# Performance work log

Hardware: AMD Instinct MI355X
Metric: run time of the kernel (lower is better)

The kernel has to match this reference:

```python
import jax, jax.numpy as jnp
import numpy as np

N_NODES = 100000
N_EDGES = 1600000
IN_F = 256
OUT_F = 128


def setup_inputs() -> dict:
    key = jax.random.key(0)
    k1, k2, k3, k4, k5, k6 = jax.random.split(key, 6)
    x = jax.random.normal(k1, (N_NODES, IN_F), dtype=jnp.float32)
    edge_row = jax.random.randint(k2, (N_EDGES,), 0, N_NODES, dtype=jnp.int32)
    edge_col = jax.random.randint(k3, (N_EDGES,), 0, N_NODES, dtype=jnp.int32)
    edge_val = jax.random.uniform(k4, (N_EDGES,), dtype=jnp.float32)
    # xavier_uniform for W: bound = sqrt(6/(fan_in+fan_out))
    bound_w = float(np.sqrt(6.0 / (IN_F + OUT_F)))
    W = jax.random.uniform(k5, (IN_F, OUT_F), dtype=jnp.float32, minval=-bound_w, maxval=bound_w)
    stdv = 1.0 / float(np.sqrt(OUT_F))
    b = jax.random.uniform(k6, (OUT_F,), dtype=jnp.float32, minval=-stdv, maxval=stdv)
    return {"x": x, "edge_row": edge_row, "edge_col": edge_col, "edge_val": edge_val, "W": W, "b": b}


def reference(x, edge_row, edge_col, edge_val, W, b):
    # dropout p=0.0 -> identity
    support = x @ W + b                      # [N, out]
    # sparse adjacency matmul: out[r] += val * support[c] over edges (r, c, val)
    msgs = edge_val[:, None] * support[edge_col]          # [E, out]
    out = jax.ops.segment_sum(msgs, edge_row, num_segments=N_NODES)  # [N, out]
    return jax.nn.relu(out)
```

## Files before the change

kernel.cpp:

```cpp
#include <hip/hip_runtime.h>


constexpr int kNodes = 100000;
constexpr int kEdges = 1600000;
constexpr int kInF   = 256;
constexpr int kOutF  = 128;
constexpr int kTiles = kNodes / 16;
constexpr int kBucketBlocks = 800;
constexpr int kGemmBlocks = 1250;

constexpr int kNB = 256;
constexpr int kRB = 391;
constexpr int kCap = 7424;
constexpr int kTileCap = 1024;

typedef __attribute__((ext_vector_type(8))) short short8;
typedef __attribute__((ext_vector_type(8))) unsigned short ush8;
typedef __attribute__((ext_vector_type(4))) float floatx4;

__device__ inline unsigned short f2bf_rne(float f) {
    unsigned int u = __float_as_uint(f);
    unsigned int r = u + 0x7FFFu + ((u >> 16) & 1u);
    return (unsigned short)(r >> 16);
}
__device__ inline float bf2f(unsigned short h) {
    return __uint_as_float(((unsigned int)h) << 16);
}

__device__ inline short8 cvt8_bf16(const float4 a, const float4 b) {
    union { short8 s; unsigned int u[4]; } r;
    asm("v_cvt_pk_bf16_f32 %0, %1, %2" : "=v"(r.u[0]) : "v"(a.x), "v"(a.y));
    asm("v_cvt_pk_bf16_f32 %0, %1, %2" : "=v"(r.u[1]) : "v"(a.z), "v"(a.w));
    asm("v_cvt_pk_bf16_f32 %0, %1, %2" : "=v"(r.u[2]) : "v"(b.x), "v"(b.y));
    asm("v_cvt_pk_bf16_f32 %0, %1, %2" : "=v"(r.u[3]) : "v"(b.z), "v"(b.w));
    return r.s;
}

__device__ inline void gload_lds16(const void* g, void* l) {
    __builtin_amdgcn_global_load_lds(
        (const __attribute__((address_space(1))) unsigned int*)g,
        (__attribute__((address_space(3))) unsigned int*)l,
        16, 0, 0);
}

__global__ __launch_bounds__(256) void gcn_gemm(const float* __restrict__ x,
                                                const float* __restrict__ W,
                                                const float* __restrict__ b,
                                                unsigned short* __restrict__ support) {
    __shared__ __align__(16) float lbuf[2][4096];

    const int lane = threadIdx.x & 63;
    const int wv   = threadIdx.x >> 6;
    const int rowl = lane & 15;
    const int quad = lane >> 4;
    const int colbase = wv * 32;

    short8 bfrag[2][8];
#pragma unroll
    for (int ct = 0; ct < 2; ++ct) {
        const int col = colbase + ct * 16 + rowl;
#pragma unroll
        for (int kc = 0; kc < 8; ++kc) {
            const int kb = kc * 32 + quad * 8;
            short8 f;
#pragma unroll
            for (int j = 0; j < 8; ++j)
                f[j] = (short)f2bf_rne(W[(size_t)(kb + j) * kOutF + col]);
            bfrag[ct][kc] = f;
        }
    }
    const float bias0 = b[colbase + rowl];
    const float bias1 = b[colbase + 16 + rowl];

    const int G = gridDim.x;
    int t = blockIdx.x;

#define GEMM_STAGE(buf_, tile_)                                                   \
    do {                                                                          \
        const float* tb_ = x + (size_t)(tile_) * 16 * kInF;                       \
        _Pragma("unroll")                                                         \
        for (int i_ = 0; i_ < 4; ++i_) {                                          \
            const int row_ = i_ * 4 + wv;                                         \
            gload_lds16(tb_ + (size_t)row_ * kInF + ((lane ^ (row_ & 7)) << 2),   \
                        &lbuf[buf_][row_ << 8]);                                  \
        }                                                                         \
    } while (0)

    if (t < kTiles) GEMM_STAGE(0, t);
    int cur = 0;

    for (; t < kTiles; t += G) {
        const int tn = t + G;
        asm volatile("s_waitcnt vmcnt(0)" ::: "memory");
        __syncthreads();
        if (tn < kTiles) GEMM_STAGE(cur ^ 1, tn);

        const int r0 = t * 16;
        const float* base = &lbuf[cur][rowl << 8];
        const int rsw = rowl & 7;
        floatx4 acc0 = {0.f, 0.f, 0.f, 0.f};
        floatx4 acc1 = {0.f, 0.f, 0.f, 0.f};
#pragma unroll
        for (int kc = 0; kc < 8; ++kc) {
            const int g0 = (kc << 3) + (quad << 1);
            const float4 v0 = *reinterpret_cast<const float4*>(base + ((g0 ^ rsw) << 2));
            const float4 v1 = *reinterpret_cast<const float4*>(base + (((g0 + 1) ^ rsw) << 2));
            const short8 a = cvt8_bf16(v0, v1);
            acc0 = __builtin_amdgcn_mfma_f32_16x16x32_bf16(a, bfrag[0][kc], acc0, 0, 0, 0);
            acc1 = __builtin_amdgcn_mfma_f32_16x16x32_bf16(a, bfrag[1][kc], acc1, 0, 0, 0);
        }
#pragma unroll
        for (int reg = 0; reg < 4; ++reg) {
            const size_t rbase = (size_t)(r0 + quad * 4 + reg) * kOutF + colbase;
            support[rbase + rowl]      = f2bf_rne(acc0[reg] + bias0);
            support[rbase + 16 + rowl] = f2bf_rne(acc1[reg] + bias1);
        }
        cur ^= 1;
    }
#undef GEMM_STAGE
}

__global__ __launch_bounds__(256) void gcn_bhist(const int* __restrict__ erow,
                                                 int* __restrict__ bucket_tot) {
    __shared__ int cnt[kNB];
    cnt[threadIdx.x] = 0;
    __syncthreads();
    const int stride = gridDim.x * blockDim.x;
    for (int e = blockIdx.x * blockDim.x + threadIdx.x; e < kEdges; e += stride)
        atomicAdd(&cnt[(unsigned int)erow[e] / (unsigned int)kRB], 1);
    __syncthreads();
    const int c = cnt[threadIdx.x];
    if (c) atomicAdd(&bucket_tot[threadIdx.x], c);
}

__global__ __launch_bounds__(256) void gcn_bscan(const int* __restrict__ bucket_tot,
                                                 int* __restrict__ bucket_base,
                                                 int* __restrict__ bucket_cursor,
                                                 int* __restrict__ row_start) {
    __shared__ int s[256];
    const int v = bucket_tot[threadIdx.x];
    s[threadIdx.x] = v;
    __syncthreads();
#pragma unroll
    for (int off = 1; off < 256; off <<= 1) {
        const int t = (threadIdx.x >= off) ? s[threadIdx.x - off] : 0;
        __syncthreads();
        s[threadIdx.x] += t;
        __syncthreads();
    }
    const int excl = s[threadIdx.x] - v;
    bucket_base[threadIdx.x]   = excl;
    bucket_cursor[threadIdx.x] = excl;
    if (threadIdx.x == 255) {
        bucket_base[256]   = kEdges;
        row_start[kNodes]  = kEdges;
    }
}

__global__ __launch_bounds__(256) void gcn_bin(const int* __restrict__ erow,
                                               const int* __restrict__ ecol,
                                               const float* __restrict__ eval,
                                               int* __restrict__ bucket_cursor,
                                               int2* __restrict__ packed) {
    __shared__ int cnt[kNB];
    __shared__ int base[kNB];
    __shared__ int rk[kNB];
    const int T   = kBucketBlocks * 256;
    const int tid = blockIdx.x * 256 + threadIdx.x;

    cnt[threadIdx.x] = 0;
    rk[threadIdx.x]  = 0;

    int bk[8], pk[8], vb[8];
    bool ok[8];
#pragma unroll
    for (int i = 0; i < 8; ++i) {
        const int e = tid + i * T;
        ok[i] = (e < kEdges);
        const int r = ok[i] ? erow[e] : 0;
        const int c = ok[i] ? ecol[e] : 0;
        const float v = ok[i] ? eval[e] : 0.f;
        const unsigned int b = (unsigned int)r / (unsigned int)kRB;
        bk[i] = (int)b;
        pk[i] = ((r - (int)b * kRB) << 17) | c;
        vb[i] = __float_as_int(v);
    }
    __syncthreads();
#pragma unroll
    for (int i = 0; i < 8; ++i)
        if (ok[i]) atomicAdd(&cnt[bk[i]], 1);
    __syncthreads();
    const int c = cnt[threadIdx.x];
    base[threadIdx.x] = c ? atomicAdd(&bucket_cursor[threadIdx.x], c) : 0;
    __syncthreads();
#pragma unroll
    for (int i = 0; i < 8; ++i) {
        if (ok[i]) {
            const int r = atomicAdd(&rk[bk[i]], 1);
            packed[base[bk[i]] + r] = make_int2(pk[i], vb[i]);
        }
    }
}

__global__ __launch_bounds__(256) void gcn_place(const int* __restrict__ bucket_base,
                                                 int* __restrict__ row_start,
                                                 int2* __restrict__ packed) {
    __shared__ int2 st[kCap];
    __shared__ int  s[512];
    __shared__ int  rcur[kRB + 1];
    const int bk = blockIdx.x;
    const int r0 = bk * kRB;
    const int r1 = min(r0 + kRB, kNodes);
    const int NR = r1 - r0;
    if (NR <= 0) return;
    const int bb = bucket_base[bk];
    const int s1 = bucket_base[bk + 1];
    const int size   = s1 - bb;
    const int staged = min(size, kCap);
    const int tid = threadIdx.x;

    s[tid] = 0;
    s[tid + 256] = 0;
    __syncthreads();

    for (int i = tid; i < staged; i += 256) {
        const int2 p = packed[bb + i];
        st[i] = p;
        atomicAdd(&s[p.x >> 17], 1);
    }
    int2 tail[8];
    int  nt = 0;
    for (int i = kCap + tid; i < size; i += 256) {
        if (nt < 8) {
            tail[nt] = packed[bb + i];
            atomicAdd(&s[tail[nt].x >> 17], 1);
            ++nt;
        }
    }
    __syncthreads();

    const int i0 = tid, i1 = tid + 256;
#pragma unroll
    for (int off = 1; off < 512; off <<= 1) {
        const int v0 = (i0 >= off) ? s[i0 - off] : 0;
        const int v1 = (i1 >= off) ? s[i1 - off] : 0;
        __syncthreads();
        s[i0] += v0;
        s[i1] += v1;
        __syncthreads();
    }

    for (int i = tid; i < NR; i += 256) {
        const int excl = i ? s[i - 1] : 0;
        row_start[r0 + i] = bb + excl;
        rcur[i] = excl;
    }
    __syncthreads();

    for (int i = tid; i < staged; i += 256) {
        const int2 p  = st[i];
        const int pos = bb + atomicAdd(&rcur[p.x >> 17], 1);
        packed[pos] = make_int2(p.x & 0x1FFFF, p.y);
    }
#pragma unroll
    for (int t = 0; t < 8; ++t) {
        if (t < nt) {
            const int2 p  = tail[t];
            const int pos = bb + atomicAdd(&rcur[p.x >> 17], 1);
            packed[pos] = make_int2(p.x & 0x1FFFF, p.y);
        }
    }
}

__global__ __launch_bounds__(256) void gcn_aggregate(const int* __restrict__ row_start,
                                                     const int2* __restrict__ packed,
                                                     const unsigned short* __restrict__ support,
                                                     float* __restrict__ out) {
    __shared__ int2 ep[kTileCap];
    const int n0 = blockIdx.x * 16;
    const int e0 = row_start[n0];
    const int eN = row_start[n0 + 16] - e0;
    const int nStage = min(eN, kTileCap);
    for (int i = threadIdx.x; i < nStage; i += 256)
        ep[i] = packed[e0 + i];
    __syncthreads();

    const int n  = n0 + (threadIdx.x >> 4);
    const int f8 = (threadIdx.x & 15) * 8;
    const unsigned short* sb = support + f8;
    const int s0 = row_start[n]     - e0;
    const int s1 = row_start[n + 1] - e0;

    float acc[8];
#pragma unroll
    for (int j = 0; j < 8; ++j) acc[j] = 0.f;

    if (eN <= kTileCap) {
        int i = s0;
        for (; i + 7 < s1; i += 8) {
            int2 p[8];
#pragma unroll
            for (int k = 0; k < 8; ++k) p[k] = ep[i + k];
            ush8 g[8];
#pragma unroll
            for (int k = 0; k < 8; ++k)
                g[k] = *reinterpret_cast<const ush8*>(sb + (size_t)p[k].x * kOutF);
#pragma unroll
            for (int k = 0; k < 8; ++k) {
                const float v = __int_as_float(p[k].y);
#pragma unroll
                for (int j = 0; j < 8; ++j) acc[j] += v * bf2f(g[k][j]);
            }
        }
        for (; i < s1; ++i) {
            const int2 p = ep[i];
            const float v = __int_as_float(p.y);
            const ush8 g = *reinterpret_cast<const ush8*>(sb + (size_t)p.x * kOutF);
#pragma unroll
            for (int j = 0; j < 8; ++j) acc[j] += v * bf2f(g[j]);
        }
    } else {
        int i = s0;
        for (; i + 3 < s1; i += 4) {
            const int2 p0 = packed[e0 + i];
            const int2 p1 = packed[e0 + i + 1];
            const int2 p2 = packed[e0 + i + 2];
            const int2 p3 = packed[e0 + i + 3];
            const ush8 a0 = *reinterpret_cast<const ush8*>(sb + (size_t)p0.x * kOutF);
            const ush8 a1 = *reinterpret_cast<const ush8*>(sb + (size_t)p1.x * kOutF);
            const ush8 a2 = *reinterpret_cast<const ush8*>(sb + (size_t)p2.x * kOutF);
            const ush8 a3 = *reinterpret_cast<const ush8*>(sb + (size_t)p3.x * kOutF);
            const float v0 = __int_as_float(p0.y), v1 = __int_as_float(p1.y);
            const float v2 = __int_as_float(p2.y), v3 = __int_as_float(p3.y);
#pragma unroll
            for (int j = 0; j < 8; ++j) {
                acc[j] += v0 * bf2f(a0[j]);
                acc[j] += v1 * bf2f(a1[j]);
                acc[j] += v2 * bf2f(a2[j]);
                acc[j] += v3 * bf2f(a3[j]);
            }
        }
        for (; i < s1; ++i) {
            const int2 p = packed[e0 + i];
            const float v = __int_as_float(p.y);
            const ush8 a = *reinterpret_cast<const ush8*>(sb + (size_t)p.x * kOutF);
#pragma unroll
            for (int j = 0; j < 8; ++j) acc[j] += v * bf2f(a[j]);
        }
    }

    float4 o0 = make_float4(fmaxf(acc[0], 0.f), fmaxf(acc[1], 0.f),
                            fmaxf(acc[2], 0.f), fmaxf(acc[3], 0.f));
    float4 o1 = make_float4(fmaxf(acc[4], 0.f), fmaxf(acc[5], 0.f),
                            fmaxf(acc[6], 0.f), fmaxf(acc[7], 0.f));
    *reinterpret_cast<float4*>(out + (size_t)n * kOutF + f8)     = o0;
    *reinterpret_cast<float4*>(out + (size_t)n * kOutF + f8 + 4) = o1;
}

extern "C" void kernel_launch(void* const* d_in, const int* in_sizes, int n_in,
                              void* d_out, int out_size, void* d_ws, size_t ws_size,
                              hipStream_t stream) {
    const float* x    = (const float*)d_in[0];
    const int*   erow = (const int*)  d_in[1];
    const int*   ecol = (const int*)  d_in[2];
    const float* eval = (const float*)d_in[3];
    const float* W    = (const float*)d_in[4];
    const float* b    = (const float*)d_in[5];
    float* out = (float*)d_out;

    char* ws = (char*)d_ws;
    unsigned short* support = (unsigned short*)(ws);
    int2* packed        = (int2*)(ws + 25600000);
    int*  row_start     = (int*) (ws + 38400000);
    int*  bucket_tot    = (int*) (ws + 38800008);
    int*  bucket_base   = (int*) (ws + 38801032);
    int*  bucket_cursor = (int*) (ws + 38802060);

    gcn_gemm<<<kGemmBlocks, 256, 0, stream>>>(x, W, b, support);

    hipMemsetAsync(bucket_tot, 0, kNB * sizeof(int), stream);
    gcn_bhist<<<1024, 256, 0, stream>>>(erow, bucket_tot);
    gcn_bscan<<<1, 256, 0, stream>>>(bucket_tot, bucket_base, bucket_cursor, row_start);
    gcn_bin  <<<kBucketBlocks, 256, 0, stream>>>(erow, ecol, eval, bucket_cursor, packed);
    gcn_place<<<kNB, 256, 0, stream>>>(bucket_base, row_start, packed);

    gcn_aggregate<<<kTiles, 256, 0, stream>>>(row_start, packed, support, out);
}
```

Baseline: 349.0 us.

## Fuse CSR build into one cooperative kernel with grid syncs and finer buckets

Replaces the four CSR-construction kernels (bucket histogram, scan, bin, place) with one cooperative kernel. It uses grid-wide syncs between the count, scatter and per-bucket placement phases, so erow is read once and kept in registers. Buckets are made finer (768 buckets of 131 rows) so each block owns one bucket and stages it in a smaller LDS buffer. This removes several launch gaps and one pass over erow, in exchange for grid.sync overhead and a requirement that all 768 blocks be co-resident.

```diff
diff --git a/kernel.cpp b/kernel.cpp
--- a/kernel.cpp
+++ b/kernel.cpp
@@ -1,4 +1,7 @@
 #include <hip/hip_runtime.h>
+#include <hip/hip_cooperative_groups.h>
+
+namespace cg = cooperative_groups;
 
 
 constexpr int kNodes = 100000;
@@ -6,12 +9,14 @@
 constexpr int kInF   = 256;
 constexpr int kOutF  = 128;
 constexpr int kTiles = kNodes / 16;
-constexpr int kBucketBlocks = 800;
 constexpr int kGemmBlocks = 1250;
 
-constexpr int kNB = 256;
-constexpr int kRB = 391;
-constexpr int kCap = 7424;
+constexpr int kNB  = 768;
+constexpr int kRB  = 131;
+constexpr int kCap = 2432;
+constexpr int kCsrBlocks = kNB;
+constexpr int kEPB = (kEdges + kCsrBlocks - 1) / kCsrBlocks;
+
 constexpr int kTileCap = 1024;
 
 typedef __attribute__((ext_vector_type(8))) short short8;
@@ -120,153 +125,131 @@
 #undef GEMM_STAGE
 }
 
-__global__ __launch_bounds__(256) void gcn_bhist(const int* __restrict__ erow,
-                                                 int* __restrict__ bucket_tot) {
-    __shared__ int cnt[kNB];
-    cnt[threadIdx.x] = 0;
-    __syncthreads();
-    const int stride = gridDim.x * blockDim.x;
-    for (int e = blockIdx.x * blockDim.x + threadIdx.x; e < kEdges; e += stride)
-        atomicAdd(&cnt[(unsigned int)erow[e] / (unsigned int)kRB], 1);
-    __syncthreads();
-    const int c = cnt[threadIdx.x];
-    if (c) atomicAdd(&bucket_tot[threadIdx.x], c);
-}
-
-__global__ __launch_bounds__(256) void gcn_bscan(const int* __restrict__ bucket_tot,
-                                                 int* __restrict__ bucket_base,
-                                                 int* __restrict__ bucket_cursor,
-                                                 int* __restrict__ row_start) {
-    __shared__ int s[256];
-    const int v = bucket_tot[threadIdx.x];
-    s[threadIdx.x] = v;
-    __syncthreads();
-#pragma unroll
-    for (int off = 1; off < 256; off <<= 1) {
-        const int t = (threadIdx.x >= off) ? s[threadIdx.x - off] : 0;
+__global__ __launch_bounds__(256, 3) void gcn_csr(const int* __restrict__ erow,
+                                                  const int* __restrict__ ecol,
+                                                  const float* __restrict__ eval,
+                                                  int* __restrict__ cursor_rel,
+                                                  int2* __restrict__ packed,
+                                                  int* __restrict__ row_start) {
+    __shared__ int2 st[kCap];
+    __shared__ int  cnt[kNB];
+    __shared__ int  rk[kNB];
+    __shared__ int  s2[kNB];
+    const int tid = threadIdx.x;
+    const int blk = blockIdx.x;
+    cg::grid_group grid = cg::this_grid();
+
+    const int eb0 = blk * kEPB;
+    const int eb1 = min(eb0 + kEPB, kEdges);
+
+    for (int i = tid; i < kNB; i += 256) { cnt[i] = 0; rk[i] = 0; }
+    __syncthreads();
+    unsigned int bkrl[9];
+#pragma unroll
+    for (int i = 0; i < 9; ++i) {
+        const int e = eb0 + i * 256 + tid;
+        bkrl[i] = 0xFFFFFFFFu;
+        if (e < eb1) {
+            const int r = erow[e];
+            const unsigned int bk = (unsigned int)r / (unsigned int)kRB;
+            bkrl[i] = (bk << 8) | (unsigned int)(r - (int)bk * kRB);
+            atomicAdd(&cnt[bk], 1);
+        }
+    }
+    __syncthreads();
+    for (int i = tid; i < kNB; i += 256) {
+        const int c = cnt[i];
+        cnt[i] = c ? atomicAdd(&cursor_rel[i], c) : 0;
+    }
+    __threadfence();
+    grid.sync();
+
+    {
+        for (int j = 0; j < 3; ++j) s2[tid + j * 256] = cursor_rel[tid + j * 256];
         __syncthreads();
-        s[threadIdx.x] += t;
-        __syncthreads();
-    }
-    const int excl = s[threadIdx.x] - v;
-    bucket_base[threadIdx.x]   = excl;
-    bucket_cursor[threadIdx.x] = excl;
-    if (threadIdx.x == 255) {
-        bucket_base[256]   = kEdges;
-        row_start[kNodes]  = kEdges;
-    }
-}
-
-__global__ __launch_bounds__(256) void gcn_bin(const int* __restrict__ erow,
-                                               const int* __restrict__ ecol,
-                                               const float* __restrict__ eval,
-                                               int* __restrict__ bucket_cursor,
-                                               int2* __restrict__ packed) {
-    __shared__ int cnt[kNB];
-    __shared__ int base[kNB];
-    __shared__ int rk[kNB];
-    const int T   = kBucketBlocks * 256;
-    const int tid = blockIdx.x * 256 + threadIdx.x;
-
-    cnt[threadIdx.x] = 0;
-    rk[threadIdx.x]  = 0;
-
-    int bk[8], pk[8], vb[8];
-    bool ok[8];
-#pragma unroll
-    for (int i = 0; i < 8; ++i) {
-        const int e = tid + i * T;
-        ok[i] = (e < kEdges);
-        const int r = ok[i] ? erow[e] : 0;
-        const int c = ok[i] ? ecol[e] : 0;
-        const float v = ok[i] ? eval[e] : 0.f;
-        const unsigned int b = (unsigned int)r / (unsigned int)kRB;
-        bk[i] = (int)b;
-        pk[i] = ((r - (int)b * kRB) << 17) | c;
-        vb[i] = __float_as_int(v);
-    }
-    __syncthreads();
-#pragma unroll
-    for (int i = 0; i < 8; ++i)
-        if (ok[i]) atomicAdd(&cnt[bk[i]], 1);
-    __syncthreads();
-    const int c = cnt[threadIdx.x];
-    base[threadIdx.x] = c ? atomicAdd(&bucket_cursor[threadIdx.x], c) : 0;
-    __syncthreads();
-#pragma unroll
-    for (int i = 0; i < 8; ++i) {
-        if (ok[i]) {
-            const int r = atomicAdd(&rk[bk[i]], 1);
-            packed[base[bk[i]] + r] = make_int2(pk[i], vb[i]);
-        }
-    }
-}
-
-__global__ __launch_bounds__(256) void gcn_place(const int* __restrict__ bucket_base,
-                                                 int* __restrict__ row_start,
-                                                 int2* __restrict__ packed) {
-    __shared__ int2 st[kCap];
-    __shared__ int  s[512];
-    __shared__ int  rcur[kRB + 1];
-    const int bk = blockIdx.x;
-    const int r0 = bk * kRB;
+        for (int off = 1; off < kNB; off <<= 1) {
+            int v0 = 0, v1 = 0, v2 = 0;
+            if (tid        >= off) v0 = s2[tid        - off];
+            if (tid + 256  >= off) v1 = s2[tid + 256  - off];
+            if (tid + 512  >= off) v2 = s2[tid + 512  - off];
+            __syncthreads();
+            s2[tid]       += v0;
+            s2[tid + 256] += v1;
+            s2[tid + 512] += v2;
+            __syncthreads();
+        }
+    }
+    const int inclb = s2[blk];
+    const int sbase = blk ? s2[blk - 1] : 0;
+    const int ssize = inclb - sbase;
+    for (int i = tid; i < kNB; i += 256)
+        cnt[i] += (i ? s2[i - 1] : 0);
+    __syncthreads();
+
+#pragma unroll
+    for (int i = 0; i < 9; ++i) {
+        const int e = eb0 + i * 256 + tid;
+        if (e < eb1) {
+            const unsigned int br = bkrl[i];
+            const int bk = (int)(br >> 8);
+            const int rl = (int)(br & 0xFFu);
+            const int c  = ecol[e];
+            const float v = eval[e];
+            const int pos = cnt[bk] + atomicAdd(&rk[bk], 1);
+            packed[pos] = make_int2((rl << 17) | c, __float_as_int(v));
+        }
+    }
+    __threadfence();
+    grid.sync();
+
+    const int r0 = blk * kRB;
+    if (r0 >= kNodes) return;
     const int r1 = min(r0 + kRB, kNodes);
     const int NR = r1 - r0;
-    if (NR <= 0) return;
-    const int bb = bucket_base[bk];
-    const int s1 = bucket_base[bk + 1];
-    const int size   = s1 - bb;
-    const int staged = min(size, kCap);
-    const int tid = threadIdx.x;
-
-    s[tid] = 0;
-    s[tid + 256] = 0;
-    __syncthreads();
-
+    const int staged = min(ssize, kCap);
+
+    s2[tid] = 0;
+    __syncthreads();
     for (int i = tid; i < staged; i += 256) {
-        const int2 p = packed[bb + i];
+        const int2 p = packed[sbase + i];
         st[i] = p;
-        atomicAdd(&s[p.x >> 17], 1);
+        atomicAdd(&s2[p.x >> 17], 1);
     }
     int2 tail[8];
     int  nt = 0;
-    for (int i = kCap + tid; i < size; i += 256) {
+    for (int i = kCap + tid; i < ssize; i += 256) {
         if (nt < 8) {
-            tail[nt] = packed[bb + i];
-            atomicAdd(&s[tail[nt].x >> 17], 1);
+            tail[nt] = packed[sbase + i];
+            atomicAdd(&s2[tail[nt].x >> 17], 1);
             ++nt;
         }
     }
     __syncthreads();
 
-    const int i0 = tid, i1 = tid + 256;
-#pragma unroll
-    for (int off = 1; off < 512; off <<= 1) {
-        const int v0 = (i0 >= off) ? s[i0 - off] : 0;
-        const int v1 = (i1 >= off) ? s[i1 - off] : 0;
+    for (int off = 1; off < 256; off <<= 1) {
+        const int v = (tid >= off) ? s2[tid - off] : 0;
         __syncthreads();
-        s[i0] += v0;
-        s[i1] += v1;
+        s2[tid] += v;
         __syncthreads();
     }
-
-    for (int i = tid; i < NR; i += 256) {
-        const int excl = i ? s[i - 1] : 0;
-        row_start[r0 + i] = bb + excl;
-        rcur[i] = excl;
-    }
+    if (tid < NR) {
+        const int excl = tid ? s2[tid - 1] : 0;
+        row_start[r0 + tid] = sbase + excl;
+        rk[tid] = excl;
+    }
+    if (blk == 0 && tid == 0) row_start[kNodes] = kEdges;
     __syncthreads();
 
     for (int i = tid; i < staged; i += 256) {
         const int2 p  = st[i];
-        const int pos = bb + atomicAdd(&rcur[p.x >> 17], 1);
+        const int pos = sbase + atomicAdd(&rk[p.x >> 17], 1);
         packed[pos] = make_int2(p.x & 0x1FFFF, p.y);
     }
 #pragma unroll
     for (int t = 0; t < 8; ++t) {
         if (t < nt) {
             const int2 p  = tail[t];
-            const int pos = bb + atomicAdd(&rcur[p.x >> 17], 1);
+            const int pos = sbase + atomicAdd(&rk[p.x >> 17], 1);
             packed[pos] = make_int2(p.x & 0x1FFFF, p.y);
         }
     }
@@ -370,19 +353,17 @@
 
     char* ws = (char*)d_ws;
     unsigned short* support = (unsigned short*)(ws);
-    int2* packed        = (int2*)(ws + 25600000);
-    int*  row_start     = (int*) (ws + 38400000);
-    int*  bucket_tot    = (int*) (ws + 38800008);
-    int*  bucket_base   = (int*) (ws + 38801032);
-    int*  bucket_cursor = (int*) (ws + 38802060);
+    int2* packed     = (int2*)(ws + 25600000);
+    int*  row_start  = (int*) (ws + 38400000);
+    int*  cursor_rel = (int*) (ws + 38800008);
 
     gcn_gemm<<<kGemmBlocks, 256, 0, stream>>>(x, W, b, support);
 
-    hipMemsetAsync(bucket_tot, 0, kNB * sizeof(int), stream);
-    gcn_bhist<<<1024, 256, 0, stream>>>(erow, bucket_tot);
-    gcn_bscan<<<1, 256, 0, stream>>>(bucket_tot, bucket_base, bucket_cursor, row_start);
-    gcn_bin  <<<kBucketBlocks, 256, 0, stream>>>(erow, ecol, eval, bucket_cursor, packed);
-    gcn_place<<<kNB, 256, 0, stream>>>(bucket_base, row_start, packed);
+    hipMemsetAsync(cursor_rel, 0, kNB * sizeof(int), stream);
+    void* cargs[] = {(void*)&erow, (void*)&ecol, (void*)&eval,
+                     (void*)&cursor_rel, (void*)&packed, (void*)&row_start};
+    hipLaunchCooperativeKernel((const void*)gcn_csr, dim3(kCsrBlocks), dim3(256),
+                               cargs, 0, stream);
 
     gcn_aggregate<<<kTiles, 256, 0, stream>>>(row_start, packed, support, out);
 }
```

New measurement: 619.6 us. +77.6%, slower.

## Use finer row buckets and contiguous per-block edge ranges in binning sort

Applied to the files above, without the earlier changes.

Increases the number of row buckets from 256 to 1024 (98 rows each), so each placement block handles a smaller bucket with a smaller shared staging area and a shorter 128-entry scan. The bin kernel now gives each of 256 blocks a contiguous edge range, makes two passes (count, then scatter) instead of holding 8 edges in registers, and reads erow twice. The aim is more parallelism and better occupancy in gcn_place and more local scatter writes, at the cost of extra global reads and more global cursor atomics.

```diff
diff --git a/kernel.cpp b/kernel.cpp
--- a/kernel.cpp
+++ b/kernel.cpp
@@ -6,12 +6,14 @@
 constexpr int kInF   = 256;
 constexpr int kOutF  = 128;
 constexpr int kTiles = kNodes / 16;
-constexpr int kBucketBlocks = 800;
 constexpr int kGemmBlocks = 1250;
 
-constexpr int kNB = 256;
-constexpr int kRB = 391;
-constexpr int kCap = 7424;
+constexpr int kNB  = 1024;
+constexpr int kRB  = 98;
+constexpr int kCap = 1792;
+constexpr int kBinBlocks = 256;
+constexpr int kEPB = kEdges / kBinBlocks;
+
 constexpr int kTileCap = 1024;
 
 typedef __attribute__((ext_vector_type(8))) short short8;
@@ -123,82 +125,87 @@
 __global__ __launch_bounds__(256) void gcn_bhist(const int* __restrict__ erow,
                                                  int* __restrict__ bucket_tot) {
     __shared__ int cnt[kNB];
-    cnt[threadIdx.x] = 0;
-    __syncthreads();
-    const int stride = gridDim.x * blockDim.x;
-    for (int e = blockIdx.x * blockDim.x + threadIdx.x; e < kEdges; e += stride)
+    const int tid = threadIdx.x;
+    for (int i = tid; i < kNB; i += 256) cnt[i] = 0;
+    __syncthreads();
+    const int eb0 = blockIdx.x * kEPB;
+    const int eb1 = min(eb0 + kEPB, kEdges);
+    for (int e = eb0 + tid; e < eb1; e += 256)
         atomicAdd(&cnt[(unsigned int)erow[e] / (unsigned int)kRB], 1);
     __syncthreads();
-    const int c = cnt[threadIdx.x];
-    if (c) atomicAdd(&bucket_tot[threadIdx.x], c);
+    for (int i = tid; i < kNB; i += 256) {
+        const int c = cnt[i];
+        if (c) atomicAdd(&bucket_tot[i], c);
+    }
 }
 
 __global__ __launch_bounds__(256) void gcn_bscan(const int* __restrict__ bucket_tot,
                                                  int* __restrict__ bucket_base,
-                                                 int* __restrict__ bucket_cursor,
+                                                 int* __restrict__ cursor,
                                                  int* __restrict__ row_start) {
-    __shared__ int s[256];
-    const int v = bucket_tot[threadIdx.x];
-    s[threadIdx.x] = v;
-    __syncthreads();
-#pragma unroll
-    for (int off = 1; off < 256; off <<= 1) {
-        const int t = (threadIdx.x >= off) ? s[threadIdx.x - off] : 0;
-        __syncthreads();
-        s[threadIdx.x] += t;
-        __syncthreads();
-    }
-    const int excl = s[threadIdx.x] - v;
-    bucket_base[threadIdx.x]   = excl;
-    bucket_cursor[threadIdx.x] = excl;
-    if (threadIdx.x == 255) {
-        bucket_base[256]   = kEdges;
-        row_start[kNodes]  = kEdges;
+    __shared__ int s[kNB];
+    const int tid = threadIdx.x;
+    int t[4];
+#pragma unroll
+    for (int j = 0; j < 4; ++j) {
+        const int idx = tid + j * 256;
+        t[j] = bucket_tot[idx];
+        s[idx] = t[j];
+    }
+    __syncthreads();
+    for (int off = 1; off < kNB; off <<= 1) {
+        int v[4];
+#pragma unroll
+        for (int j = 0; j < 4; ++j) {
+            const int idx = tid + j * 256;
+            v[j] = (idx >= off) ? s[idx - off] : 0;
+        }
+        __syncthreads();
+#pragma unroll
+        for (int j = 0; j < 4; ++j) s[tid + j * 256] += v[j];
+        __syncthreads();
+    }
+#pragma unroll
+    for (int j = 0; j < 4; ++j) {
+        const int idx = tid + j * 256;
+        const int excl = s[idx] - t[j];
+        bucket_base[idx] = excl;
+        cursor[idx]      = excl;
+    }
+    if (tid == 255) {
+        bucket_base[kNB]  = kEdges;
+        row_start[kNodes] = kEdges;
     }
 }
 
 __global__ __launch_bounds__(256) void gcn_bin(const int* __restrict__ erow,
                                                const int* __restrict__ ecol,
                                                const float* __restrict__ eval,
-                                               int* __restrict__ bucket_cursor,
+                                               int* __restrict__ cursor,
                                                int2* __restrict__ packed) {
     __shared__ int cnt[kNB];
-    __shared__ int base[kNB];
     __shared__ int rk[kNB];
-    const int T   = kBucketBlocks * 256;
-    const int tid = blockIdx.x * 256 + threadIdx.x;
-
-    cnt[threadIdx.x] = 0;
-    rk[threadIdx.x]  = 0;
-
-    int bk[8], pk[8], vb[8];
-    bool ok[8];
-#pragma unroll
-    for (int i = 0; i < 8; ++i) {
-        const int e = tid + i * T;
-        ok[i] = (e < kEdges);
-        const int r = ok[i] ? erow[e] : 0;
-        const int c = ok[i] ? ecol[e] : 0;
-        const float v = ok[i] ? eval[e] : 0.f;
-        const unsigned int b = (unsigned int)r / (unsigned int)kRB;
-        bk[i] = (int)b;
-        pk[i] = ((r - (int)b * kRB) << 17) | c;
-        vb[i] = __float_as_int(v);
-    }
-    __syncthreads();
-#pragma unroll
-    for (int i = 0; i < 8; ++i)
-        if (ok[i]) atomicAdd(&cnt[bk[i]], 1);
-    __syncthreads();
-    const int c = cnt[threadIdx.x];
-    base[threadIdx.x] = c ? atomicAdd(&bucket_cursor[threadIdx.x], c) : 0;
-    __syncthreads();
-#pragma unroll
-    for (int i = 0; i < 8; ++i) {
-        if (ok[i]) {
-            const int r = atomicAdd(&rk[bk[i]], 1);
-            packed[base[bk[i]] + r] = make_int2(pk[i], vb[i]);
-        }
+    const int tid = threadIdx.x;
+    const int eb0 = blockIdx.x * kEPB;
+    const int eb1 = min(eb0 + kEPB, kEdges);
+    for (int i = tid; i < kNB; i += 256) { cnt[i] = 0; rk[i] = 0; }
+    __syncthreads();
+#pragma unroll 4
+    for (int e = eb0 + tid; e < eb1; e += 256)
+        atomicAdd(&cnt[(unsigned int)erow[e] / (unsigned int)kRB], 1);
+    __syncthreads();
+    for (int i = tid; i < kNB; i += 256) {
+        const int c = cnt[i];
+        cnt[i] = c ? atomicAdd(&cursor[i], c) : 0;
+    }
+    __syncthreads();
+#pragma unroll 4
+    for (int e = eb0 + tid; e < eb1; e += 256) {
+        const int r = erow[e];
+        const unsigned int bk = (unsigned int)r / (unsigned int)kRB;
+        const int rl = r - (int)bk * kRB;
+        const int pos = cnt[bk] + atomicAdd(&rk[bk], 1);
+        packed[pos] = make_int2((rl << 17) | ecol[e], __float_as_int(eval[e]));
     }
 }
 
@@ -206,21 +213,20 @@
                                                  int* __restrict__ row_start,
                                                  int2* __restrict__ packed) {
     __shared__ int2 st[kCap];
-    __shared__ int  s[512];
-    __shared__ int  rcur[kRB + 1];
+    __shared__ int  s[128];
+    __shared__ int  rcur[kRB];
     const int bk = blockIdx.x;
     const int r0 = bk * kRB;
+    if (r0 >= kNodes) return;
     const int r1 = min(r0 + kRB, kNodes);
     const int NR = r1 - r0;
-    if (NR <= 0) return;
     const int bb = bucket_base[bk];
     const int s1 = bucket_base[bk + 1];
     const int size   = s1 - bb;
     const int staged = min(size, kCap);
     const int tid = threadIdx.x;
 
-    s[tid] = 0;
-    s[tid + 256] = 0;
+    if (tid < 128) s[tid] = 0;
     __syncthreads();
 
     for (int i = tid; i < staged; i += 256) {
@@ -239,21 +245,17 @@
     }
     __syncthreads();
 
-    const int i0 = tid, i1 = tid + 256;
-#pragma unroll
-    for (int off = 1; off < 512; off <<= 1) {
-        const int v0 = (i0 >= off) ? s[i0 - off] : 0;
-        const int v1 = (i1 >= off) ? s[i1 - off] : 0;
-        __syncthreads();
-        s[i0] += v0;
-        s[i1] += v1;
-        __syncthreads();
-    }
-
-    for (int i = tid; i < NR; i += 256) {
-        const int excl = i ? s[i - 1] : 0;
-        row_start[r0 + i] = bb + excl;
-        rcur[i] = excl;
+    for (int off = 1; off < 128; off <<= 1) {
+        int v = 0;
+        if (tid < 128 && tid >= off) v = s[tid - off];
+        __syncthreads();
+        if (tid < 128) s[tid] += v;
+        __syncthreads();
+    }
+    if (tid < NR) {
+        const int excl = tid ? s[tid - 1] : 0;
+        row_start[r0 + tid] = bb + excl;
+        rcur[tid] = excl;
     }
     __syncthreads();
 
@@ -370,18 +372,18 @@
 
     char* ws = (char*)d_ws;
     unsigned short* support = (unsigned short*)(ws);
-    int2* packed        = (int2*)(ws + 25600000);
-    int*  row_start     = (int*) (ws + 38400000);
-    int*  bucket_tot    = (int*) (ws + 38800008);
-    int*  bucket_base   = (int*) (ws + 38801032);
-    int*  bucket_cursor = (int*) (ws + 38802060);
+    int2* packed      = (int2*)(ws + 25600000);
+    int*  row_start   = (int*) (ws + 38400000);
+    int*  bucket_tot  = (int*) (ws + 38800008);
+    int*  bucket_base = (int*) (ws + 38804104);
+    int*  cursor      = (int*) (ws + 38808204);
 
     gcn_gemm<<<kGemmBlocks, 256, 0, stream>>>(x, W, b, support);
 
     hipMemsetAsync(bucket_tot, 0, kNB * sizeof(int), stream);
-    gcn_bhist<<<1024, 256, 0, stream>>>(erow, bucket_tot);
-    gcn_bscan<<<1, 256, 0, stream>>>(bucket_tot, bucket_base, bucket_cursor, row_start);
-    gcn_bin  <<<kBucketBlocks, 256, 0, stream>>>(erow, ecol, eval, bucket_cursor, packed);
+    gcn_bhist<<<kBinBlocks, 256, 0, stream>>>(erow, bucket_tot);
+    gcn_bscan<<<1, 256, 0, stream>>>(bucket_tot, bucket_base, cursor, row_start);
+    gcn_bin  <<<kBinBlocks, 256, 0, stream>>>(erow, ecol, eval, cursor, packed);
     gcn_place<<<kNB, 256, 0, stream>>>(bucket_base, row_start, packed);
 
     gcn_aggregate<<<kTiles, 256, 0, stream>>>(row_start, packed, support, out);
```

New measurement: 331.5 us. -5.0%, faster.
